# Kernel optimization log

Measured on AMD Instinct MI355X. Metric: run time of the kernel, lower is better.

The kernel has to match this reference:

```python
import jax, jax.numpy as jnp
import numpy as np
import math

B, T, C = 4, 2048, 1024
NH = 16
HS = C // NH

def setup_inputs() -> dict:
    key = jax.random.key(0)
    ks = jax.random.split(key, 5)
    s = 0.02
    return {
        "x": jax.random.normal(ks[0], (B, T, C), dtype=jnp.float32),
        "W_attn": jax.random.normal(ks[1], (C, 3 * C), dtype=jnp.float32) * s,
        "b_attn": jax.random.normal(ks[2], (3 * C,), dtype=jnp.float32) * s,
        "W_proj": jax.random.normal(ks[3], (C, C), dtype=jnp.float32) * s,
        "b_proj": jax.random.normal(ks[4], (C,), dtype=jnp.float32) * s,
    }

def reference(x, W_attn, b_attn, W_proj, b_proj):
    Bx, Tx, Cx = x.shape
    qkv = x @ W_attn + b_attn                      # [B,T,3C]
    q, k, v = jnp.split(qkv, 3, axis=-1)
    # [B,T,C] -> [B,nh,T,hs]
    def heads(t):
        return t.reshape(Bx, Tx, NH, HS).transpose(0, 2, 1, 3)
    q, k, v = heads(q), heads(k), heads(v)
    att = jnp.einsum('bhqd,bhkd->bhqk', q, k) * (1.0 / math.sqrt(HS))
    causal = jnp.tril(jnp.ones((Tx, Tx), dtype=bool))
    att = jnp.where(causal[None, None], att, -jnp.inf)
    att = jax.nn.softmax(att, axis=-1)
    y = jnp.einsum('bhqk,bhkd->bhqd', att, v)      # [B,nh,T,hs]
    y = y.transpose(0, 2, 1, 3).reshape(Bx, Tx, Cx)
    return y @ W_proj + b_proj
```

## Files before the change

### kernel.cpp

```cpp
#include <hip/hip_runtime.h>
#include <hip/hip_bf16.h>
#include <stdint.h>

typedef __bf16 bf16x8 __attribute__((ext_vector_type(8)));
typedef __bf16 bf16x4 __attribute__((ext_vector_type(4)));
typedef float  f32x4  __attribute__((ext_vector_type(4)));

#define MFMA16(a, b, c) __builtin_amdgcn_mfma_f32_16x16x32_bf16((a), (b), (c), 0, 0, 0)

constexpr int BATCH = 4;
constexpr int TSEQ  = 2048;
constexpr int CDIM  = 1024;
constexpr int NHEAD = 16;
constexpr int HSZ   = 64;
constexpr size_t HEADELEMS = (size_t)BATCH * NHEAD * TSEQ * HSZ;

constexpr int LDF = 72;

__device__ __forceinline__ void load_lds_128(const __bf16* g, __bf16* l) {
    __builtin_amdgcn_global_load_lds(
        (const __attribute__((address_space(1))) unsigned int*)g,
        (__attribute__((address_space(3))) unsigned int*)l,
        16, 0, 0);
}

__global__ void conv_f32_bf16(const float* __restrict__ src, __bf16* __restrict__ dst, int n)
{
    const int i0 = (blockIdx.x * 256 + threadIdx.x) * 8;
    if (i0 >= n) return;
    float4 a = *(const float4*)(src + i0);
    float4 b = *(const float4*)(src + i0 + 4);
    bf16x8 o;
    o[0] = (__bf16)a.x; o[1] = (__bf16)a.y; o[2] = (__bf16)a.z; o[3] = (__bf16)a.w;
    o[4] = (__bf16)b.x; o[5] = (__bf16)b.y; o[6] = (__bf16)b.z; o[7] = (__bf16)b.w;
    *(bf16x8*)(dst + i0) = o;
}

__global__ void conv_transpose_bf16(const float* __restrict__ src, __bf16* __restrict__ dst,
                                    int K, int N)
{
    __shared__ __bf16 tile[32][33];
    const int n0 = blockIdx.x * 32, k0 = blockIdx.y * 32;
    const int tx = threadIdx.x & 31, ty = threadIdx.x >> 5;
    #pragma unroll
    for (int i = 0; i < 32; i += 8)
        tile[ty + i][tx] = (__bf16)src[(size_t)(k0 + ty + i) * N + n0 + tx];
    __syncthreads();
    #pragma unroll
    for (int i = 0; i < 32; i += 8)
        dst[(size_t)(n0 + ty + i) * K + k0 + tx] = tile[tx][ty + i];
}

__global__ __launch_bounds__(256, 3)
void gemm_bt_pipe(const __bf16* __restrict__ A, const __bf16* __restrict__ BT,
                  const float* __restrict__ bias, __bf16* __restrict__ outp,
                  int M, int N, int K)
{
    __shared__ __bf16 As[3][128 * 32];
    __shared__ __bf16 Bs[3][128 * 32];

    const int t    = threadIdx.x;
    const int wave = t >> 6, lane = t & 63;
    const int quad = lane >> 4, l16 = lane & 15;
    const int bm = blockIdx.y * 128, bn = blockIdx.x * 128;
    const int wm = (wave >> 1) * 64, wn = (wave & 1) * 64;

    const int lrow = lane >> 2, lchunk = lane & 3;

    f32x4 acc[4][4];
    #pragma unroll
    for (int i = 0; i < 4; ++i)
        #pragma unroll
        for (int j = 0; j < 4; ++j)
            acc[i][j] = (f32x4){0.f, 0.f, 0.f, 0.f};

    const int c0 = wave * 2, c1 = wave * 2 + 1;
    const __bf16* a0 = A  + (size_t)(bm + 16 * c0 + lrow) * K + 8 * lchunk;
    const __bf16* a1 = A  + (size_t)(bm + 16 * c1 + lrow) * K + 8 * lchunk;
    const __bf16* b0 = BT + (size_t)(bn + 16 * c0 + lrow) * K + 8 * lchunk;
    const __bf16* b1 = BT + (size_t)(bn + 16 * c1 + lrow) * K + 8 * lchunk;

    const int nk = K >> 5;

#define STAGE(buf, kofs) do { \
    load_lds_128(a0 + (kofs), &As[buf][c0 * 512]); \
    load_lds_128(a1 + (kofs), &As[buf][c1 * 512]); \
    load_lds_128(b0 + (kofs), &Bs[buf][c0 * 512]); \
    load_lds_128(b1 + (kofs), &Bs[buf][c1 * 512]); } while (0)

    STAGE(0, 0);
    if (nk > 1) STAGE(1, 32);

    int cur = 0;
    for (int it = 0; it < nk; ++it) {
        if (it + 1 < nk) asm volatile("s_waitcnt vmcnt(4)" ::: "memory");
        else             asm volatile("s_waitcnt vmcnt(0)" ::: "memory");
        __builtin_amdgcn_s_barrier();
        __builtin_amdgcn_sched_barrier(0);

        if (it + 2 < nk) {
            const int stg = (cur >= 1) ? cur - 1 : cur + 2;
            STAGE(stg, (it + 2) * 32);
        }

        bf16x8 af[4], bfr[4];
        #pragma unroll
        for (int i = 0; i < 4; ++i)
            af[i]  = *(const bf16x8*)(&As[cur][(wm + i * 16 + l16) * 32 + quad * 8]);
        #pragma unroll
        for (int i = 0; i < 4; ++i)
            bfr[i] = *(const bf16x8*)(&Bs[cur][(wn + i * 16 + l16) * 32 + quad * 8]);
        #pragma unroll
        for (int mi = 0; mi < 4; ++mi)
            #pragma unroll
            for (int ni = 0; ni < 4; ++ni)
                acc[mi][ni] = MFMA16(af[mi], bfr[ni], acc[mi][ni]);

        cur = (cur + 1 >= 3) ? 0 : cur + 1;
    }
#undef STAGE

    #pragma unroll
    for (int ni = 0; ni < 4; ++ni) {
        const int col = bn + wn + ni * 16 + l16;
        const float bv = bias[col];
        const int which = col >> 10;
        const int c = col & 1023;
        const int h = c >> 6, d = c & 63;
        #pragma unroll
        for (int mi = 0; mi < 4; ++mi)
            #pragma unroll
            for (int r = 0; r < 4; ++r) {
                const int row = bm + wm + mi * 16 + quad * 4 + r;
                const int bb = row >> 11, tt = row & 2047;
                size_t idx;
                if (which == 2)
                    idx = 2 * HEADELEMS + ((((size_t)bb * NHEAD + h) * HSZ + d) * TSEQ + tt);
                else
                    idx = (size_t)which * HEADELEMS
                        + ((((size_t)bb * NHEAD + h) * TSEQ + tt) * HSZ + d);
                outp[idx] = (__bf16)(acc[mi][ni][r] + bv);
            }
    }
}

__global__ __launch_bounds__(256, 4)
void gemm_bt_proj(const __bf16* __restrict__ A, const __bf16* __restrict__ BT,
                  const float* __restrict__ bias, float* __restrict__ outp,
                  int M, int N, int K)
{
    __shared__ __bf16 As[2][128 * 32];
    __shared__ __bf16 Bs[2][128 * 32];

    const int t    = threadIdx.x;
    const int wave = t >> 6, lane = t & 63;
    const int quad = lane >> 4, l16 = lane & 15;
    const int bm = blockIdx.y * 128, bn = blockIdx.x * 128;
    const int wm = (wave >> 1) * 64, wn = (wave & 1) * 64;

    const int lrow = lane >> 2, lchunk = lane & 3;

    f32x4 acc[4][4];
    #pragma unroll
    for (int i = 0; i < 4; ++i)
        #pragma unroll
        for (int j = 0; j < 4; ++j)
            acc[i][j] = (f32x4){0.f, 0.f, 0.f, 0.f};

    const int c0 = wave * 2, c1 = wave * 2 + 1;
    const __bf16* a0 = A  + (size_t)(bm + 16 * c0 + lrow) * K + 8 * lchunk;
    const __bf16* a1 = A  + (size_t)(bm + 16 * c1 + lrow) * K + 8 * lchunk;
    const __bf16* b0 = BT + (size_t)(bn + 16 * c0 + lrow) * K + 8 * lchunk;
    const __bf16* b1 = BT + (size_t)(bn + 16 * c1 + lrow) * K + 8 * lchunk;

    const int nk = K >> 5;
    load_lds_128(a0, &As[0][c0 * 512]);
    load_lds_128(a1, &As[0][c1 * 512]);
    load_lds_128(b0, &Bs[0][c0 * 512]);
    load_lds_128(b1, &Bs[0][c1 * 512]);

    for (int it = 0; it < nk; ++it) {
        asm volatile("s_waitcnt vmcnt(0)" ::: "memory");
        __syncthreads();
        const int cur = it & 1, nxt = cur ^ 1;
        if (it + 1 < nk) {
            const int k0 = (it + 1) * 32;
            load_lds_128(a0 + k0, &As[nxt][c0 * 512]);
            load_lds_128(a1 + k0, &As[nxt][c1 * 512]);
            load_lds_128(b0 + k0, &Bs[nxt][c0 * 512]);
            load_lds_128(b1 + k0, &Bs[nxt][c1 * 512]);
        }

        bf16x8 af[4], bfr[4];
        #pragma unroll
        for (int i = 0; i < 4; ++i)
            af[i]  = *(const bf16x8*)(&As[cur][(wm + i * 16 + l16) * 32 + quad * 8]);
        #pragma unroll
        for (int i = 0; i < 4; ++i)
            bfr[i] = *(const bf16x8*)(&Bs[cur][(wn + i * 16 + l16) * 32 + quad * 8]);
        #pragma unroll
        for (int mi = 0; mi < 4; ++mi)
            #pragma unroll
            for (int ni = 0; ni < 4; ++ni)
                acc[mi][ni] = MFMA16(af[mi], bfr[ni], acc[mi][ni]);
    }

    #pragma unroll
    for (int ni = 0; ni < 4; ++ni) {
        const int col = bn + wn + ni * 16 + l16;
        const float bv = bias[col];
        #pragma unroll
        for (int mi = 0; mi < 4; ++mi)
            #pragma unroll
            for (int r = 0; r < 4; ++r) {
                const int row = bm + wm + mi * 16 + quad * 4 + r;
                outp[(size_t)row * N + col] = acc[mi][ni][r] + bv;
            }
    }
}

__global__ __launch_bounds__(256, 4)
void flash_attn(const __bf16* __restrict__ Q, const __bf16* __restrict__ Kg,
                const __bf16* __restrict__ Vg, __bf16* __restrict__ Y)
{
    __shared__ __bf16 Ks[64 * LDF];
    __shared__ __bf16 Vs[64 * LDF];
    __shared__ __bf16 Ps[4][32 * LDF];

    const int t = threadIdx.x, wave = t >> 6, lane = t & 63;
    const int quad = lane >> 4, l16 = lane & 15;
    const int bh = blockIdx.x;
    const size_t base = (size_t)bh * TSEQ * HSZ;
    const int b = bh >> 4, h = bh & 15;

    const float sc = 0.125f * 1.44269504088896341f;

    bf16x8 ones;
    #pragma unroll
    for (int j = 0; j < 8; ++j) ones[j] = (__bf16)1.0f;

    const int s_row = t >> 2, s_c16 = (t & 3) * 16;

    for (int half = 0; half < 2; ++half) {
        const int qt = half ? 15 - (int)blockIdx.y : (int)blockIdx.y;
        const int q0 = qt * 128;

        bf16x8 qf[2][2];
        #pragma unroll
        for (int mi = 0; mi < 2; ++mi) {
            const int qrow = q0 + wave * 32 + mi * 16 + l16;
            #pragma unroll
            for (int hh = 0; hh < 2; ++hh) {
                bf16x8 raw = *(const bf16x8*)(Q + base + (size_t)qrow * HSZ + hh * 32 + quad * 8);
                #pragma unroll
                for (int j = 0; j < 8; ++j) qf[mi][hh][j] = (__bf16)((float)raw[j] * sc);
            }
        }

        f32x4 oacc[2][4];
        f32x4 lacc[2];
        #pragma unroll
        for (int mi = 0; mi < 2; ++mi) {
            lacc[mi] = (f32x4){0.f, 0.f, 0.f, 0.f};
            #pragma unroll
            for (int dt = 0; dt < 4; ++dt) oacc[mi][dt] = (f32x4){0.f, 0.f, 0.f, 0.f};
        }

        const int iters = q0 / 64 + 2;
        for (int it = 0; it < iters; ++it) {
            const int kt = it * 64;
            {
                const __bf16* kp = Kg + base + (size_t)(kt + s_row) * HSZ + s_c16;
                bf16x8 v0 = *(const bf16x8*)kp;
                bf16x8 v1 = *(const bf16x8*)(kp + 8);
                *(bf16x8*)(&Ks[s_row * LDF + s_c16])     = v0;
                *(bf16x8*)(&Ks[s_row * LDF + s_c16 + 8]) = v1;
            }
            {
                const __bf16* vp = Vg + base + (size_t)s_row * TSEQ + kt + s_c16;
                bf16x8 v0 = *(const bf16x8*)vp;
                bf16x8 v1 = *(const bf16x8*)(vp + 8);
                *(bf16x8*)(&Vs[s_row * LDF + s_c16])     = v0;
                *(bf16x8*)(&Vs[s_row * LDF + s_c16 + 8]) = v1;
            }
            __syncthreads();

            const bool active = (kt <= q0 + wave * 32 + 31);
            if (active) {
                f32x4 st[4][2];
                #pragma unroll
                for (int ktl = 0; ktl < 4; ++ktl) {
                    bf16x8 kf0 = *(const bf16x8*)(&Ks[(ktl * 16 + l16) * LDF + quad * 8]);
                    bf16x8 kf1 = *(const bf16x8*)(&Ks[(ktl * 16 + l16) * LDF + 32 + quad * 8]);
                    #pragma unroll
                    for (int mi = 0; mi < 2; ++mi) {
                        f32x4 a = (f32x4){0.f, 0.f, 0.f, 0.f};
                        a = MFMA16(kf0, qf[mi][0], a);
                        a = MFMA16(kf1, qf[mi][1], a);
                        st[ktl][mi] = a;
                    }
                }

                if (kt + 63 >= q0 + wave * 32) {
                    #pragma unroll
                    for (int ktl = 0; ktl < 4; ++ktl)
                        #pragma unroll
                        for (int mi = 0; mi < 2; ++mi)
                            #pragma unroll
                            for (int r = 0; r < 4; ++r) {
                                const int key = kt + ktl * 16 + quad * 4 + r;
                                const int qr  = q0 + wave * 32 + mi * 16 + l16;
                                if (key > qr) st[ktl][mi][r] = -1e30f;
                            }
                }

                #pragma unroll
                for (int ktl = 0; ktl < 4; ++ktl)
                    #pragma unroll
                    for (int mi = 0; mi < 2; ++mi) {
                        bf16x4 pv;
                        #pragma unroll
                        for (int r = 0; r < 4; ++r)
                            pv[r] = (__bf16)exp2f(st[ktl][mi][r]);
                        *(bf16x4*)(&Ps[wave][(mi * 16 + l16) * LDF + ktl * 16 + quad * 4]) = pv;
                    }

                asm volatile("s_waitcnt lgkmcnt(0)" ::: "memory");

                bf16x8 pf[2][2];
                #pragma unroll
                for (int mi = 0; mi < 2; ++mi) {
                    pf[mi][0] = *(const bf16x8*)(&Ps[wave][(mi * 16 + l16) * LDF + quad * 8]);
                    pf[mi][1] = *(const bf16x8*)(&Ps[wave][(mi * 16 + l16) * LDF + 32 + quad * 8]);
                    lacc[mi] = MFMA16(pf[mi][0], ones, lacc[mi]);
                    lacc[mi] = MFMA16(pf[mi][1], ones, lacc[mi]);
                }
                #pragma unroll
                for (int dt = 0; dt < 4; ++dt) {
                    bf16x8 vf0 = *(const bf16x8*)(&Vs[(dt * 16 + l16) * LDF + quad * 8]);
                    bf16x8 vf1 = *(const bf16x8*)(&Vs[(dt * 16 + l16) * LDF + 32 + quad * 8]);
                    #pragma unroll
                    for (int mi = 0; mi < 2; ++mi) {
                        oacc[mi][dt] = MFMA16(pf[mi][0], vf0, oacc[mi][dt]);
                        oacc[mi][dt] = MFMA16(pf[mi][1], vf1, oacc[mi][dt]);
                    }
                }
            }
            __syncthreads();
        }

        #pragma unroll
        for (int mi = 0; mi < 2; ++mi) {
            const f32x4 linv = {1.f / lacc[mi][0], 1.f / lacc[mi][1],
                                1.f / lacc[mi][2], 1.f / lacc[mi][3]};
            #pragma unroll
            for (int dt = 0; dt < 4; ++dt)
                #pragma unroll
                for (int r = 0; r < 4; ++r) {
                    const int tt = q0 + wave * 32 + mi * 16 + quad * 4 + r;
                    const int d  = dt * 16 + l16;
                    Y[((size_t)(b * TSEQ + tt) * CDIM) + h * HSZ + d] =
                        (__bf16)(oacc[mi][dt][r] * linv[r]);
                }
        }
    }
}

extern "C" void kernel_launch(void* const* d_in, const int* in_sizes, int n_in,
                              void* d_out, int out_size, void* d_ws, size_t ws_size,
                              hipStream_t stream)
{
    const int NX = 8388608, NWA = 3145728, NWP = 1048576;
    char* wsb = (char*)d_ws;

    size_t off = 0;
    __bf16* cx   = (__bf16*)(wsb + off); off += (size_t)2 * NX;
    __bf16* cwaT = (__bf16*)(wsb + off); off += (size_t)2 * NWA;
    __bf16* cwpT = (__bf16*)(wsb + off); off += (size_t)2 * NWP;
    __bf16* q    = (__bf16*)(wsb + off);
    __bf16* y    = q + 3 * HEADELEMS;

    const float* xf = (const float*)d_in[0];
    const float* ba = (const float*)d_in[2];
    const float* bp = (const float*)d_in[4];

    conv_f32_bf16<<<NX / 2048, 256, 0, stream>>>(xf, cx, NX);
    conv_transpose_bf16<<<dim3(3 * CDIM / 32, CDIM / 32), 256, 0, stream>>>(
        (const float*)d_in[1], cwaT, CDIM, 3 * CDIM);
    conv_transpose_bf16<<<dim3(CDIM / 32, CDIM / 32), 256, 0, stream>>>(
        (const float*)d_in[3], cwpT, CDIM, CDIM);

    gemm_bt_pipe<<<dim3(3 * CDIM / 128, BATCH * TSEQ / 128), 256, 0, stream>>>(
        cx, cwaT, ba, q, BATCH * TSEQ, 3 * CDIM, CDIM);

    flash_attn<<<dim3(BATCH * NHEAD, 8), 256, 0, stream>>>(
        q, q + HEADELEMS, q + 2 * HEADELEMS, y);

    gemm_bt_proj<<<dim3(CDIM / 128, BATCH * TSEQ / 128), 256, 0, stream>>>(
        y, cwpT, bp, (float*)d_out, BATCH * TSEQ, CDIM, CDIM);
}
```

Measured before the change: 277.6 us.

## Split long causal query tiles across two blocks with a combine kernel

Result: slower. 288.1 us (+3.8%).

```diff
diff --git a/kernel.cpp b/kernel.cpp
--- a/kernel.cpp
+++ b/kernel.cpp
@@ -220,8 +220,9 @@
 }
 
 __global__ __launch_bounds__(256, 4)
-void flash_attn(const __bf16* __restrict__ Q, const __bf16* __restrict__ Kg,
-                const __bf16* __restrict__ Vg, __bf16* __restrict__ Y)
+void flash_attn_sp(const __bf16* __restrict__ Q, const __bf16* __restrict__ Kg,
+                   const __bf16* __restrict__ Vg, __bf16* __restrict__ Y,
+                   float* __restrict__ Opart, float* __restrict__ lpart)
 {
     __shared__ __bf16 Ks[64 * LDF];
     __shared__ __bf16 Vs[64 * LDF];
@@ -231,124 +232,127 @@
     const int quad = lane >> 4, l16 = lane & 15;
     const int bh = blockIdx.x;
     const size_t base = (size_t)bh * TSEQ * HSZ;
-    const int b = bh >> 4, h = bh & 15;
+
+    const int u = blockIdx.y, j = u / 3, m = u - 3 * j;
+    const bool split = (m < 2);
+    int qt, it0, it1;
+    if (split) { qt = 15 - j; const int h0 = qt + 1; it0 = m ? h0 : 0; it1 = m ? 2 * qt + 2 : h0; }
+    else       { qt = 7 - j;  it0 = 0; it1 = 2 * qt + 2; }
+    const int q0 = qt * 128;
 
     const float sc = 0.125f * 1.44269504088896341f;
 
+    bf16x8 qf[2][2];
+    #pragma unroll
+    for (int mi = 0; mi < 2; ++mi) {
+        const int qrow = q0 + wave * 32 + mi * 16 + l16;
+        #pragma unroll
+        for (int hh = 0; hh < 2; ++hh) {
+            bf16x8 raw = *(const bf16x8*)(Q + base + (size_t)qrow * HSZ + hh * 32 + quad * 8);
+            #pragma unroll
+            for (int jj = 0; jj < 8; ++jj) qf[mi][hh][jj] = (__bf16)((float)raw[jj] * sc);
+        }
+    }
+
     bf16x8 ones;
     #pragma unroll
-    for (int j = 0; j < 8; ++j) ones[j] = (__bf16)1.0f;
+    for (int jj = 0; jj < 8; ++jj) ones[jj] = (__bf16)1.0f;
+
+    f32x4 oacc[2][4];
+    f32x4 lacc[2];
+    #pragma unroll
+    for (int mi = 0; mi < 2; ++mi) {
+        lacc[mi] = (f32x4){0.f, 0.f, 0.f, 0.f};
+        #pragma unroll
+        for (int dt = 0; dt < 4; ++dt) oacc[mi][dt] = (f32x4){0.f, 0.f, 0.f, 0.f};
+    }
 
     const int s_row = t >> 2, s_c16 = (t & 3) * 16;
 
-    for (int half = 0; half < 2; ++half) {
-        const int qt = half ? 15 - (int)blockIdx.y : (int)blockIdx.y;
-        const int q0 = qt * 128;
-
-        bf16x8 qf[2][2];
-        #pragma unroll
-        for (int mi = 0; mi < 2; ++mi) {
-            const int qrow = q0 + wave * 32 + mi * 16 + l16;
-            #pragma unroll
-            for (int hh = 0; hh < 2; ++hh) {
-                bf16x8 raw = *(const bf16x8*)(Q + base + (size_t)qrow * HSZ + hh * 32 + quad * 8);
-                #pragma unroll
-                for (int j = 0; j < 8; ++j) qf[mi][hh][j] = (__bf16)((float)raw[j] * sc);
-            }
-        }
-
-        f32x4 oacc[2][4];
-        f32x4 lacc[2];
-        #pragma unroll
-        for (int mi = 0; mi < 2; ++mi) {
-            lacc[mi] = (f32x4){0.f, 0.f, 0.f, 0.f};
-            #pragma unroll
-            for (int dt = 0; dt < 4; ++dt) oacc[mi][dt] = (f32x4){0.f, 0.f, 0.f, 0.f};
-        }
-
-        const int iters = q0 / 64 + 2;
-        for (int it = 0; it < iters; ++it) {
-            const int kt = it * 64;
-            {
-                const __bf16* kp = Kg + base + (size_t)(kt + s_row) * HSZ + s_c16;
-                bf16x8 v0 = *(const bf16x8*)kp;
-                bf16x8 v1 = *(const bf16x8*)(kp + 8);
-                *(bf16x8*)(&Ks[s_row * LDF + s_c16])     = v0;
-                *(bf16x8*)(&Ks[s_row * LDF + s_c16 + 8]) = v1;
-            }
-            {
-                const __bf16* vp = Vg + base + (size_t)s_row * TSEQ + kt + s_c16;
-                bf16x8 v0 = *(const bf16x8*)vp;
-                bf16x8 v1 = *(const bf16x8*)(vp + 8);
-                *(bf16x8*)(&Vs[s_row * LDF + s_c16])     = v0;
-                *(bf16x8*)(&Vs[s_row * LDF + s_c16 + 8]) = v1;
-            }
-            __syncthreads();
-
-            const bool active = (kt <= q0 + wave * 32 + 31);
-            if (active) {
-                f32x4 st[4][2];
-                #pragma unroll
-                for (int ktl = 0; ktl < 4; ++ktl) {
-                    bf16x8 kf0 = *(const bf16x8*)(&Ks[(ktl * 16 + l16) * LDF + quad * 8]);
-                    bf16x8 kf1 = *(const bf16x8*)(&Ks[(ktl * 16 + l16) * LDF + 32 + quad * 8]);
-                    #pragma unroll
-                    for (int mi = 0; mi < 2; ++mi) {
-                        f32x4 a = (f32x4){0.f, 0.f, 0.f, 0.f};
-                        a = MFMA16(kf0, qf[mi][0], a);
-                        a = MFMA16(kf1, qf[mi][1], a);
-                        st[ktl][mi] = a;
-                    }
+    for (int it = it0; it < it1; ++it) {
+        const int kt = it * 64;
+        {
+            const __bf16* kp = Kg + base + (size_t)(kt + s_row) * HSZ + s_c16;
+            bf16x8 v0 = *(const bf16x8*)kp;
+            bf16x8 v1 = *(const bf16x8*)(kp + 8);
+            *(bf16x8*)(&Ks[s_row * LDF + s_c16])     = v0;
+            *(bf16x8*)(&Ks[s_row * LDF + s_c16 + 8]) = v1;
+        }
+        {
+            const __bf16* vp = Vg + base + (size_t)s_row * TSEQ + kt + s_c16;
+            bf16x8 v0 = *(const bf16x8*)vp;
+            bf16x8 v1 = *(const bf16x8*)(vp + 8);
+            *(bf16x8*)(&Vs[s_row * LDF + s_c16])     = v0;
+            *(bf16x8*)(&Vs[s_row * LDF + s_c16 + 8]) = v1;
+        }
+        __syncthreads();
+
+        const bool active = (kt <= q0 + wave * 32 + 31);
+        if (active) {
+            f32x4 st[4][2];
+            #pragma unroll
+            for (int ktl = 0; ktl < 4; ++ktl) {
+                bf16x8 kf0 = *(const bf16x8*)(&Ks[(ktl * 16 + l16) * LDF + quad * 8]);
+                bf16x8 kf1 = *(const bf16x8*)(&Ks[(ktl * 16 + l16) * LDF + 32 + quad * 8]);
+                #pragma unroll
+                for (int mi = 0; mi < 2; ++mi) {
+                    f32x4 a = (f32x4){0.f, 0.f, 0.f, 0.f};
+                    a = MFMA16(kf0, qf[mi][0], a);
+                    a = MFMA16(kf1, qf[mi][1], a);
+                    st[ktl][mi] = a;
                 }
-
-                if (kt + 63 >= q0 + wave * 32) {
-                    #pragma unroll
-                    for (int ktl = 0; ktl < 4; ++ktl)
-                        #pragma unroll
-                        for (int mi = 0; mi < 2; ++mi)
-                            #pragma unroll
-                            for (int r = 0; r < 4; ++r) {
-                                const int key = kt + ktl * 16 + quad * 4 + r;
-                                const int qr  = q0 + wave * 32 + mi * 16 + l16;
-                                if (key > qr) st[ktl][mi][r] = -1e30f;
-                            }
-                }
-
+            }
+
+            if (kt + 63 >= q0 + wave * 32) {
                 #pragma unroll
                 for (int ktl = 0; ktl < 4; ++ktl)
                     #pragma unroll
-                    for (int mi = 0; mi < 2; ++mi) {
-                        bf16x4 pv;
+                    for (int mi = 0; mi < 2; ++mi)
                         #pragma unroll
-                        for (int r = 0; r < 4; ++r)
-                            pv[r] = (__bf16)exp2f(st[ktl][mi][r]);
-                        *(bf16x4*)(&Ps[wave][(mi * 16 + l16) * LDF + ktl * 16 + quad * 4]) = pv;
-                    }
-
-                asm volatile("s_waitcnt lgkmcnt(0)" ::: "memory");
-
-                bf16x8 pf[2][2];
+                        for (int r = 0; r < 4; ++r) {
+                            const int key = kt + ktl * 16 + quad * 4 + r;
+                            const int qr  = q0 + wave * 32 + mi * 16 + l16;
+                            if (key > qr) st[ktl][mi][r] = -1e30f;
+                        }
+            }
+
+            #pragma unroll
+            for (int ktl = 0; ktl < 4; ++ktl)
                 #pragma unroll
                 for (int mi = 0; mi < 2; ++mi) {
-                    pf[mi][0] = *(const bf16x8*)(&Ps[wave][(mi * 16 + l16) * LDF + quad * 8]);
-                    pf[mi][1] = *(const bf16x8*)(&Ps[wave][(mi * 16 + l16) * LDF + 32 + quad * 8]);
-                    lacc[mi] = MFMA16(pf[mi][0], ones, lacc[mi]);
-                    lacc[mi] = MFMA16(pf[mi][1], ones, lacc[mi]);
+                    bf16x4 pv;
+                    #pragma unroll
+                    for (int r = 0; r < 4; ++r)
+                        pv[r] = (__bf16)exp2f(st[ktl][mi][r]);
+                    *(bf16x4*)(&Ps[wave][(mi * 16 + l16) * LDF + ktl * 16 + quad * 4]) = pv;
                 }
-                #pragma unroll
-                for (int dt = 0; dt < 4; ++dt) {
-                    bf16x8 vf0 = *(const bf16x8*)(&Vs[(dt * 16 + l16) * LDF + quad * 8]);
-                    bf16x8 vf1 = *(const bf16x8*)(&Vs[(dt * 16 + l16) * LDF + 32 + quad * 8]);
-                    #pragma unroll
-                    for (int mi = 0; mi < 2; ++mi) {
-                        oacc[mi][dt] = MFMA16(pf[mi][0], vf0, oacc[mi][dt]);
-                        oacc[mi][dt] = MFMA16(pf[mi][1], vf1, oacc[mi][dt]);
-                    }
+
+            asm volatile("s_waitcnt lgkmcnt(0)" ::: "memory");
+
+            bf16x8 pf[2][2];
+            #pragma unroll
+            for (int mi = 0; mi < 2; ++mi) {
+                pf[mi][0] = *(const bf16x8*)(&Ps[wave][(mi * 16 + l16) * LDF + quad * 8]);
+                pf[mi][1] = *(const bf16x8*)(&Ps[wave][(mi * 16 + l16) * LDF + 32 + quad * 8]);
+                lacc[mi] = MFMA16(pf[mi][0], ones, lacc[mi]);
+                lacc[mi] = MFMA16(pf[mi][1], ones, lacc[mi]);
+            }
+            #pragma unroll
+            for (int dt = 0; dt < 4; ++dt) {
+                bf16x8 vf0 = *(const bf16x8*)(&Vs[(dt * 16 + l16) * LDF + quad * 8]);
+                bf16x8 vf1 = *(const bf16x8*)(&Vs[(dt * 16 + l16) * LDF + 32 + quad * 8]);
+                #pragma unroll
+                for (int mi = 0; mi < 2; ++mi) {
+                    oacc[mi][dt] = MFMA16(pf[mi][0], vf0, oacc[mi][dt]);
+                    oacc[mi][dt] = MFMA16(pf[mi][1], vf1, oacc[mi][dt]);
                 }
             }
-            __syncthreads();
-        }
-
+        }
+        __syncthreads();
+    }
+
+    if (!split) {
+        const int b = bh >> 4, h = bh & 15;
         #pragma unroll
         for (int mi = 0; mi < 2; ++mi) {
             const f32x4 linv = {1.f / lacc[mi][0], 1.f / lacc[mi][1],
@@ -363,6 +367,60 @@
                         (__bf16)(oacc[mi][dt][r] * linv[r]);
                 }
         }
+    } else {
+        float* Op = Opart + ((((size_t)m * 64 + bh) * 8 + (qt - 8)) * 128) * 64;
+        float* lp = lpart + (((size_t)m * 64 + bh) * 8 + (qt - 8)) * 128;
+        #pragma unroll
+        for (int mi = 0; mi < 2; ++mi) {
+            #pragma unroll
+            for (int dt = 0; dt < 4; ++dt)
+                #pragma unroll
+                for (int r = 0; r < 4; ++r) {
+                    const int row = wave * 32 + mi * 16 + quad * 4 + r;
+                    Op[(size_t)row * 64 + dt * 16 + l16] = oacc[mi][dt][r];
+                }
+            if (l16 == 0) {
+                #pragma unroll
+                for (int r = 0; r < 4; ++r)
+                    lp[wave * 32 + mi * 16 + quad * 4 + r] = lacc[mi][r];
+            }
+        }
+    }
+}
+
+__global__ __launch_bounds__(256)
+void combine_norm(const float* __restrict__ Opart, const float* __restrict__ lpart,
+                  __bf16* __restrict__ Y)
+{
+    const int bh = blockIdx.x, qt8 = blockIdx.y, t = threadIdx.x;
+    const int qt = 8 + qt8, q0 = qt * 128;
+    const int row = t >> 1, ch = (t & 1) * 32;
+
+    const size_t o0 = ((((size_t)0 * 64 + bh) * 8 + qt8) * 128 + row) * 64 + ch;
+    const size_t o1 = ((((size_t)1 * 64 + bh) * 8 + qt8) * 128 + row) * 64 + ch;
+    const float l0 = lpart[(((size_t)0 * 64 + bh) * 8 + qt8) * 128 + row];
+    const float l1 = lpart[(((size_t)1 * 64 + bh) * 8 + qt8) * 128 + row];
+    const float inv = 1.f / (l0 + l1);
+
+    const int b = bh >> 4, h = bh & 15;
+    __bf16* yp = Y + ((size_t)(b * TSEQ + q0 + row) * CDIM) + h * HSZ + ch;
+
+    #pragma unroll
+    for (int j = 0; j < 4; ++j) {
+        float4 a0 = *(const float4*)(Opart + o0 + j * 8);
+        float4 a1 = *(const float4*)(Opart + o0 + j * 8 + 4);
+        float4 b0 = *(const float4*)(Opart + o1 + j * 8);
+        float4 b1 = *(const float4*)(Opart + o1 + j * 8 + 4);
+        bf16x8 o;
+        o[0] = (__bf16)((a0.x + b0.x) * inv);
+        o[1] = (__bf16)((a0.y + b0.y) * inv);
+        o[2] = (__bf16)((a0.z + b0.z) * inv);
+        o[3] = (__bf16)((a0.w + b0.w) * inv);
+        o[4] = (__bf16)((a1.x + b1.x) * inv);
+        o[5] = (__bf16)((a1.y + b1.y) * inv);
+        o[6] = (__bf16)((a1.z + b1.z) * inv);
+        o[7] = (__bf16)((a1.w + b1.w) * inv);
+        *(bf16x8*)(yp + j * 8) = o;
     }
 }
 
@@ -379,6 +437,8 @@
     __bf16* cwpT = (__bf16*)(wsb + off); off += (size_t)2 * NWP;
     __bf16* q    = (__bf16*)(wsb + off);
     __bf16* y    = q + 3 * HEADELEMS;
+    float*  Opart = (float*)(y + HEADELEMS);
+    float*  lpart = Opart + (size_t)2 * 64 * 8 * 128 * 64;
 
     const float* xf = (const float*)d_in[0];
     const float* ba = (const float*)d_in[2];
@@ -393,8 +453,10 @@
     gemm_bt_pipe<<<dim3(3 * CDIM / 128, BATCH * TSEQ / 128), 256, 0, stream>>>(
         cx, cwaT, ba, q, BATCH * TSEQ, 3 * CDIM, CDIM);
 
-    flash_attn<<<dim3(BATCH * NHEAD, 8), 256, 0, stream>>>(
-        q, q + HEADELEMS, q + 2 * HEADELEMS, y);
+    flash_attn_sp<<<dim3(BATCH * NHEAD, 24), 256, 0, stream>>>(
+        q, q + HEADELEMS, q + 2 * HEADELEMS, y, Opart, lpart);
+
+    combine_norm<<<dim3(BATCH * NHEAD, 8), 256, 0, stream>>>(Opart, lpart, y);
 
     gemm_bt_proj<<<dim3(CDIM / 128, BATCH * TSEQ / 128), 256, 0, stream>>>(
         y, cwpT, bp, (float*)d_out, BATCH * TSEQ, CDIM, CDIM);
```
